# Performance work log

Hardware: AMD Instinct MI355X
Metric: run time of the kernel (lower is better)

The kernel has to match this reference:

```python
import jax, jax.numpy as jnp
import numpy as np

EMBED_DIM = 2048
NUM_HEADS = 32
NUM_KV_HEADS = 8
HEAD_DIM = EMBED_DIM // NUM_HEADS  # 64
KV_DIM = HEAD_DIM * NUM_KV_HEADS   # 512
Q_PER_KV = NUM_HEADS // NUM_KV_HEADS  # 4


def setup_inputs() -> dict:
    key = jax.random.key(0)
    ks = jax.random.split(key, 9)
    s = 1.0 / np.sqrt(EMBED_DIM)
    x = jax.random.normal(ks[0], (2, 2048, EMBED_DIM), dtype=jnp.float32)
    Wq = jax.random.uniform(ks[1], (EMBED_DIM, EMBED_DIM), jnp.float32, -s, s)
    bq = jax.random.uniform(ks[2], (EMBED_DIM,), jnp.float32, -s, s)
    Wk = jax.random.uniform(ks[3], (KV_DIM, EMBED_DIM), jnp.float32, -s, s)
    bk = jax.random.uniform(ks[4], (KV_DIM,), jnp.float32, -s, s)
    Wv = jax.random.uniform(ks[5], (KV_DIM, EMBED_DIM), jnp.float32, -s, s)
    bv = jax.random.uniform(ks[6], (KV_DIM,), jnp.float32, -s, s)
    Wo = jax.random.uniform(ks[7], (EMBED_DIM, EMBED_DIM), jnp.float32, -s, s)
    bo = jax.random.uniform(ks[8], (EMBED_DIM,), jnp.float32, -s, s)
    return {"x": x, "Wq": Wq, "bq": bq, "Wk": Wk, "bk": bk,
            "Wv": Wv, "bv": bv, "Wo": Wo, "bo": bo}


def reference(x, Wq, bq, Wk, bk, Wv, bv, Wo, bo):
    B, S, E = x.shape
    # projections (torch Linear: x @ W.T + b)
    q = x @ Wq.T + bq                       # [B,S,E]
    k = x @ Wk.T + bk                       # [B,S,KV_DIM]
    v = x @ Wv.T + bv
    # [B, num_kv, q_per_kv, S, D] and [B, num_kv, S, D] -- GQA grouping
    # avoids repeat_interleave duplication while computing identical math
    q = q.reshape(B, S, NUM_KV_HEADS, Q_PER_KV, HEAD_DIM).transpose(0, 2, 3, 1, 4)
    k = k.reshape(B, S, NUM_KV_HEADS, HEAD_DIM).transpose(0, 2, 1, 3)
    v = v.reshape(B, S, NUM_KV_HEADS, HEAD_DIM).transpose(0, 2, 1, 3)
    scale = 1.0 / np.sqrt(HEAD_DIM).astype(np.float32)
    scores = jnp.einsum('bgqsd,bgtd->bgqst', q, k) * scale  # [B,G,Qpk,S,S]
    causal = jnp.triu(jnp.ones((S, S), dtype=bool), k=1)
    scores = jnp.where(causal, jnp.float32(-jnp.inf), scores)
    attn = jax.nn.softmax(scores, axis=-1)
    out = jnp.einsum('bgqst,bgtd->bgqsd', attn, v)          # [B,G,Qpk,S,D]
    # back to [B,S,E]: head order matches repeat_interleave (kv-major)
    out = out.transpose(0, 3, 1, 2, 4).reshape(B, S, E)
    return out @ Wo.T + bo
```

## Files before the change

kernel.cpp:

```cpp
#include <hip/hip_runtime.h>
#include <stdint.h>

#define EMBED  2048
#define SEQ    2048
#define BATCH  2
#define NHEADS 32
#define NKV    8
#define HDIM   64
#define KVD    512
#define MTOT   (BATCH*SEQ)
#define QKVN   (EMBED + 2*KVD)

typedef __bf16 bf16x8 __attribute__((ext_vector_type(8)));
typedef float  f32x4  __attribute__((ext_vector_type(4)));
typedef float  f32x8v __attribute__((ext_vector_type(8)));
typedef float  f32x2v __attribute__((ext_vector_type(2)));
typedef float  f32x16 __attribute__((ext_vector_type(16)));

#define QSCALE 0.18033688f
#define M2     11.541560f

static __device__ __forceinline__ unsigned short f2bf(float f) {
    union { float f; unsigned int u; } v; v.f = f;
    return (unsigned short)((v.u + 0x7fffu + ((v.u >> 16) & 1u)) >> 16);
}

static __device__ __forceinline__ void gload_lds16(const void* g, void* l) {
    __builtin_amdgcn_global_load_lds(
        (const __attribute__((address_space(1))) void*)g,
        (__attribute__((address_space(3))) void*)l, 16, 0, 0);
}

template<int N> static __device__ __forceinline__ void waitvm() {
    if constexpr (N == 2) asm volatile("s_waitcnt vmcnt(2)" ::: "memory");
    else if constexpr (N == 3) asm volatile("s_waitcnt vmcnt(3)" ::: "memory");
    else asm volatile("s_waitcnt vmcnt(4)" ::: "memory");
}

static __device__ __forceinline__ void cast4(const float* __restrict__ in,
                                             unsigned short* __restrict__ out, int i) {
    float4 f = reinterpret_cast<const float4*>(in)[i];
    ushort4 o;
    o.x = f2bf(f.x); o.y = f2bf(f.y); o.z = f2bf(f.z); o.w = f2bf(f.w);
    reinterpret_cast<ushort4*>(out)[i] = o;
}

__global__ __launch_bounds__(256)
void prep(const float* __restrict__ x,  const float* __restrict__ Wq,
          const float* __restrict__ Wk, const float* __restrict__ Wv,
          const float* __restrict__ Wo, const float* __restrict__ bq,
          const float* __restrict__ bk, const float* __restrict__ bv,
          unsigned short* __restrict__ xb, unsigned short* __restrict__ Wqkvb,
          unsigned short* __restrict__ Wob, float* __restrict__ bqkv)
{
    const int t0 = blockIdx.x * blockDim.x + threadIdx.x;
    const int st = gridDim.x * blockDim.x;
    for (int i = t0; i < (MTOT * EMBED) / 4;  i += st) cast4(x,  xb, i);
    for (int i = t0; i < (EMBED * EMBED) / 4; i += st) cast4(Wq, Wqkvb, i);
    for (int i = t0; i < (KVD * EMBED) / 4;   i += st) cast4(Wk, Wqkvb + EMBED * EMBED, i);
    for (int i = t0; i < (KVD * EMBED) / 4;   i += st) cast4(Wv, Wqkvb + (EMBED + KVD) * EMBED, i);
    for (int i = t0; i < (EMBED * EMBED) / 4; i += st) cast4(Wo, Wob, i);
    if (t0 < QKVN / 4) {
        float4 v = (t0 < EMBED / 4) ? reinterpret_cast<const float4*>(bq)[t0]
                 : (t0 < (EMBED + KVD) / 4) ? reinterpret_cast<const float4*>(bk)[t0 - EMBED / 4]
                 : reinterpret_cast<const float4*>(bv)[t0 - (EMBED + KVD) / 4];
        reinterpret_cast<float4*>(bqkv)[t0] = v;
    }
}

__global__ __launch_bounds__(256)
void transpose_v(const unsigned short* __restrict__ qkv,
                 unsigned short* __restrict__ vt)
{
    __shared__ __align__(16) unsigned short T[64][72];
    const int bg = blockIdx.x & 15;
    const int bt = blockIdx.x >> 4;
    const int b  = bg >> 3, g = bg & 7;
    const int tid = threadIdx.x;
    const int tr  = tid >> 2, c = tid & 3;

    const unsigned short* src = qkv + ((size_t)(b * SEQ + bt * 64 + tr)) * QKVN
                              + (EMBED + KVD) + g * HDIM + c * 16;
    uint4 v0 = *reinterpret_cast<const uint4*>(src);
    uint4 v1 = *reinterpret_cast<const uint4*>(src + 8);
    *reinterpret_cast<uint4*>(&T[tr][c * 16])     = v0;
    *reinterpret_cast<uint4*>(&T[tr][c * 16 + 8]) = v1;
    __syncthreads();

    const int dr = tr;
    unsigned short o[16];
#pragma unroll
    for (int j = 0; j < 16; ++j) o[j] = T[c * 16 + j][dr];
    unsigned short* dst = vt + ((size_t)(bg * 64 + dr)) * SEQ + bt * 64 + c * 16;
    *reinterpret_cast<uint4*>(dst)     = *reinterpret_cast<uint4*>(o);
    *reinterpret_cast<uint4*>(dst + 8) = *reinterpret_cast<uint4*>(o + 8);
}

template<int WM, bool OUT_BF16>
__global__ __launch_bounds__(512, 1)
void gemm8p(const unsigned short* __restrict__ A,
            const unsigned short* __restrict__ B,
            const float* __restrict__ bias,
            void* __restrict__ C, int M, int N, int K)
{
    constexpr int BM    = WM * 32;
    constexpr int ASZ   = BM * 128;
    constexpr int BSZ   = 256 * 128;
    constexpr int AHALF = ASZ / 2;
    constexpr int AL    = AHALF / 8192;
    constexpr int BUFSZ = ASZ + BSZ;

    __shared__ __align__(16) char lds[2 * BUFSZ];

    const int tid = threadIdx.x;
    const int l   = tid & 63;
    const int w   = tid >> 6;
    const int wr  = w >> 2, wc = w & 3;
    const int lr15 = l & 15;
    const int lkb  = (l >> 4) * 16;

    const int nwg = gridDim.x;
    const int cpx = nwg >> 3;
    const int bid = blockIdx.x;
    const int swz = (bid & 7) * cpx + (bid >> 3);
    const int NMB = M / BM;
    const int m0  = (swz % NMB) * BM;
    const int n0  = (swz / NMB) * 256;

    unsigned offA[2][AL], dA[2][AL];
#pragma unroll
    for (int q = 0; q < 2; ++q)
#pragma unroll
        for (int j = 0; j < AL; ++j) {
            int L  = q * AHALF + (tid + j * 512) * 16;
            int R  = L >> 7;
            int cb = (L & 127) ^ ((R & 7) << 4);
            int lrow;
            if constexpr (WM == 8) lrow = ((R >> 6) & 1) * 128 + (R >> 7) * 64 + (R & 63);
            else                   lrow = ((R >> 5) & 1) * 64  + (R >> 6) * 32 + (R & 31);
            offA[q][j] = (unsigned)((m0 + lrow) * K * 2 + cb);
            dA[q][j]   = (unsigned)L;
        }
    unsigned offB[2][2], dB[2][2];
#pragma unroll
    for (int q = 0; q < 2; ++q)
#pragma unroll
        for (int j = 0; j < 2; ++j) {
            int L  = q * 16384 + (tid + j * 512) * 16;
            int R  = L >> 7;
            int cb = (L & 127) ^ ((R & 7) << 4);
            int lrow = ((R >> 5) & 3) * 64 + (R >> 7) * 32 + (R & 31);
            offB[q][j] = (unsigned)((n0 + lrow) * K * 2 + cb);
            dB[q][j]   = (unsigned)(ASZ + L);
        }

#define STAGE_A(q, bw, ku) { _Pragma("unroll") \
    for (int j_ = 0; j_ < AL; ++j_) \
        gload_lds16((const char*)A + offA[q][j_] + (unsigned)(ku) * 128u, (bw) + dA[q][j_]); }
#define STAGE_B(q, bw, ku) { _Pragma("unroll") \
    for (int j_ = 0; j_ < 2; ++j_) \
        gload_lds16((const char*)B + offB[q][j_] + (unsigned)(ku) * 128u, (bw) + dB[q][j_]); }

    auto rdA = [&](const char* br, int mi, int kk) -> bf16x8 {
        int row;
        if constexpr (WM == 8) row = (mi >> 2) * 128 + wr * 64 + (mi & 3) * 16 + lr15;
        else                   row = (mi >> 1) * 64  + wr * 32 + (mi & 1) * 16 + lr15;
        int byte = (row * 128 + kk * 64 + lkb) ^ ((row & 7) << 4);
        return *reinterpret_cast<const bf16x8*>(br + byte);
    };
    auto rdB = [&](const char* br, int ni, int kk) -> bf16x8 {
        int row  = (ni >> 1) * 128 + wc * 32 + (ni & 1) * 16 + lr15;
        int byte = (row * 128 + kk * 64 + lkb) ^ ((row & 7) << 4);
        return *reinterpret_cast<const bf16x8*>(br + ASZ + byte);
    };

    f32x4 acc[WM][4] = {};
    bf16x8 afr[WM / 2][2], bf0[2][2], bf1[2][2];

    STAGE_A(0, lds, 0); STAGE_B(0, lds, 0); STAGE_B(1, lds, 0); STAGE_A(1, lds, 0);
    waitvm<2 + AL>();
    __builtin_amdgcn_s_barrier();

    const int NKT = K >> 6;
    for (int u = 0; u < NKT; ++u) {
        char* br = lds + (u & 1) * BUFSZ;
        char* bw = lds + ((u & 1) ^ 1) * BUFSZ;
        const bool pf = (u + 1 < NKT);
        const int  ku = u + 1;

        if (pf) STAGE_A(0, bw, ku);
#pragma unroll
        for (int mi = 0; mi < WM / 2; ++mi)
#pragma unroll
            for (int kk = 0; kk < 2; ++kk) afr[mi][kk] = rdA(br, mi, kk);
#pragma unroll
        for (int ni = 0; ni < 2; ++ni)
#pragma unroll
            for (int kk = 0; kk < 2; ++kk) bf0[ni][kk] = rdB(br, ni, kk);
        __builtin_amdgcn_s_barrier();
        __builtin_amdgcn_s_setprio(1);
#pragma unroll
        for (int mi = 0; mi < WM / 2; ++mi)
#pragma unroll
            for (int ni = 0; ni < 2; ++ni)
#pragma unroll
                for (int kk = 0; kk < 2; ++kk)
                    acc[mi][ni] = __builtin_amdgcn_mfma_f32_16x16x32_bf16(afr[mi][kk], bf0[ni][kk], acc[mi][ni], 0, 0, 0);
        __builtin_amdgcn_s_setprio(0);
        waitvm<2 * AL>();
        __builtin_amdgcn_s_barrier();

        if (pf) STAGE_B(0, bw, ku);
#pragma unroll
        for (int ni = 0; ni < 2; ++ni)
#pragma unroll
            for (int kk = 0; kk < 2; ++kk) bf1[ni][kk] = rdB(br, 2 + ni, kk);
        __builtin_amdgcn_s_barrier();
        __builtin_amdgcn_s_setprio(1);
#pragma unroll
        for (int mi = 0; mi < WM / 2; ++mi)
#pragma unroll
            for (int ni = 0; ni < 2; ++ni)
#pragma unroll
                for (int kk = 0; kk < 2; ++kk)
                    acc[mi][2 + ni] = __builtin_amdgcn_mfma_f32_16x16x32_bf16(afr[mi][kk], bf1[ni][kk], acc[mi][2 + ni], 0, 0, 0);
        __builtin_amdgcn_s_setprio(0);
        waitvm<AL + 2>();
        __builtin_amdgcn_s_barrier();

        if (pf) STAGE_B(1, bw, ku);
#pragma unroll
        for (int mi = 0; mi < WM / 2; ++mi)
#pragma unroll
            for (int kk = 0; kk < 2; ++kk) afr[mi][kk] = rdA(br, WM / 2 + mi, kk);
        __builtin_amdgcn_s_barrier();
        __builtin_amdgcn_s_setprio(1);
#pragma unroll
        for (int mi = 0; mi < WM / 2; ++mi)
#pragma unroll
            for (int ni = 0; ni < 2; ++ni)
#pragma unroll
                for (int kk = 0; kk < 2; ++kk)
                    acc[WM / 2 + mi][ni] = __builtin_amdgcn_mfma_f32_16x16x32_bf16(afr[mi][kk], bf0[ni][kk], acc[WM / 2 + mi][ni], 0, 0, 0);
        __builtin_amdgcn_s_setprio(0);
        __builtin_amdgcn_s_barrier();

        if (pf) STAGE_A(1, bw, ku);
        __builtin_amdgcn_s_barrier();
        __builtin_amdgcn_s_setprio(1);
#pragma unroll
        for (int mi = 0; mi < WM / 2; ++mi)
#pragma unroll
            for (int ni = 0; ni < 2; ++ni)
#pragma unroll
                for (int kk = 0; kk < 2; ++kk)
                    acc[WM / 2 + mi][2 + ni] = __builtin_amdgcn_mfma_f32_16x16x32_bf16(afr[mi][kk], bf1[ni][kk], acc[WM / 2 + mi][2 + ni], 0, 0, 0);
        __builtin_amdgcn_s_setprio(0);
        waitvm<2 + AL>();
        __builtin_amdgcn_s_barrier();
    }
#undef STAGE_A
#undef STAGE_B

    float bv[4];
#pragma unroll
    for (int ni = 0; ni < 4; ++ni) bv[ni] = bias[n0 + wc * 64 + ni * 16 + lr15];
#pragma unroll
    for (int mi = 0; mi < WM; ++mi)
#pragma unroll
        for (int ni = 0; ni < 4; ++ni)
#pragma unroll
            for (int r = 0; r < 4; ++r) {
                int row = m0 + wr * (WM * 16) + mi * 16 + (l >> 4) * 4 + r;
                int col = n0 + wc * 64 + ni * 16 + lr15;
                float v = acc[mi][ni][r] + bv[ni];
                if constexpr (OUT_BF16)
                    ((unsigned short*)C)[(size_t)row * N + col] = f2bf(v);
                else
                    ((float*)C)[(size_t)row * N + col] = v;
            }
}

static __device__ __forceinline__ bf16x8 pack_frag(float p0, float p1, float p2, float p3,
                                                   float p4, float p5, float p6, float p7) {
    unsigned int w0, w1, w2, w3;
    asm("v_cvt_pk_bf16_f32 %0, %1, %2" : "=v"(w0) : "v"(p0), "v"(p1));
    asm("v_cvt_pk_bf16_f32 %0, %1, %2" : "=v"(w1) : "v"(p2), "v"(p3));
    asm("v_cvt_pk_bf16_f32 %0, %1, %2" : "=v"(w2) : "v"(p4), "v"(p5));
    asm("v_cvt_pk_bf16_f32 %0, %1, %2" : "=v"(w3) : "v"(p6), "v"(p7));
    asm("v_permlane32_swap_b32 %0, %1" : "+v"(w0), "+v"(w2));
    asm("v_permlane32_swap_b32 %0, %1" : "+v"(w1), "+v"(w3));
    union { unsigned int u[4]; bf16x8 v; } uu;
    uu.u[0] = w0; uu.u[1] = w1; uu.u[2] = w2; uu.u[3] = w3;
    return uu.v;
}

static __device__ __forceinline__ float hsum32(f32x16 a, f32x16 b) {
    f32x16 t = a + b;
    f32x8v u = __builtin_shufflevector(t, t, 0,1,2,3,4,5,6,7)
             + __builtin_shufflevector(t, t, 8,9,10,11,12,13,14,15);
    f32x4 v4 = __builtin_shufflevector(u, u, 0,1,2,3)
             + __builtin_shufflevector(u, u, 4,5,6,7);
    f32x2v v2 = __builtin_shufflevector(v4, v4, 0,1)
              + __builtin_shufflevector(v4, v4, 2,3);
    return v2[0] + v2[1];
}

__global__ __launch_bounds__(256, 2)
void gqa_attn(const unsigned short* __restrict__ qkv,
              const unsigned short* __restrict__ vtg,
              unsigned short* __restrict__ ctx)
{
    __shared__ __align__(16) unsigned short Ks[2][64 * 64];
    __shared__ __align__(16) unsigned short Vs[2][64 * 64];

    const int bid = blockIdx.x;
    const int g   = bid & 7;
    const int bh  = (bid >> 3) & 3;
    const int b   = bh >> 1;
    const int hp  = bh & 1;
    const int qt  = 31 - (bid >> 5);
    const int NT  = qt + 1;

    const int tid = threadIdx.x;
    const int l   = tid & 63;
    const int w   = tid >> 6;
    const int hi  = l >> 5;
    const int lq  = l & 31;

    const int h   = g * 4 + hp * 2 + (w >> 1);
    const int q0  = qt * 64 + (w & 1) * 32;
    const size_t rowb = (size_t)b * SEQ;
    const int kbase = EMBED + g * HDIM;

    bf16x8 qf[4];
    {
        const char* qa = (const char*)qkv + ((rowb + q0 + lq) * QKVN + (size_t)h * HDIM) * 2;
#pragma unroll
        for (int ks = 0; ks < 4; ++ks) {
            bf16x8 ta = *reinterpret_cast<const bf16x8*>(qa + (ks * 16 + hi * 8) * 2);
#pragma unroll
            for (int j = 0; j < 8; ++j)
                ta[j] = (__bf16)((float)ta[j] * QSCALE);
            qf[ks] = ta;
        }
    }

    f32x16 acc0 = {}, acc1 = {};
    float l_run = 0.0f;

    const int Lk0 = tid << 4;
    const int Lk1 = (tid + 256) << 4;
    const int Tk0 = Lk0 ^ (((Lk0 >> 7) & 7) << 4);
    const int Tk1 = Lk1 ^ (((Lk1 >> 7) & 7) << 4);
    const int kr0 = Tk0 >> 7, ko0 = Tk0 & 127;
    const int kr1 = Tk1 >> 7, ko1 = Tk1 & 127;

    const char* vtb = (const char*)vtg + (size_t)(b * 8 + g) * HDIM * SEQ * 2;

#define STAGE_KV(buf, tt) { \
    gload_lds16((const char*)qkv + ((rowb + (tt) + kr0) * QKVN + kbase) * 2 + ko0, (char*)Ks[buf] + Lk0); \
    gload_lds16((const char*)qkv + ((rowb + (tt) + kr1) * QKVN + kbase) * 2 + ko1, (char*)Ks[buf] + Lk1); \
    gload_lds16(vtb + ((size_t)kr0 * SEQ + (tt)) * 2 + ko0, (char*)Vs[buf] + Lk0); \
    gload_lds16(vtb + ((size_t)kr1 * SEQ + (tt)) * 2 + ko1, (char*)Vs[buf] + Lk1); }

    STAGE_KV(0, 0);
    __syncthreads();

    for (int kt = 0; kt < NT; ++kt) {
        const int cur = kt & 1;
        const int t0  = kt * 64;
        const bool haveNext = (kt + 1 < NT);
        if (haveNext) STAGE_KV(cur ^ 1, t0 + 64);

        const char* KsBuf = (const char*)Ks[cur];
        f32x16 s0 = {}, s1 = {};
        __builtin_amdgcn_s_setprio(1);
#pragma unroll
        for (int ks = 0; ks < 4; ++ks) {
            const int colb = (ks * 16 + hi * 8) * 2;
            int a0 = (lq * 128 + colb) ^ ((lq & 7) << 4);
            bf16x8 kf0 = *reinterpret_cast<const bf16x8*>(KsBuf + a0);
            s0 = __builtin_amdgcn_mfma_f32_32x32x16_bf16(kf0, qf[ks], s0, 0, 0, 0);
            int r1 = 32 + lq;
            int a1 = (r1 * 128 + colb) ^ ((r1 & 7) << 4);
            bf16x8 kf1 = *reinterpret_cast<const bf16x8*>(KsBuf + a1);
            s1 = __builtin_amdgcn_mfma_f32_32x32x16_bf16(kf1, qf[ks], s1, 0, 0, 0);
        }
        __builtin_amdgcn_s_setprio(0);

        if (kt == qt) {
            const int q = q0 + lq;
#pragma unroll
            for (int r = 0; r < 16; ++r) {
                int tg = t0 + (r & 3) + 8 * (r >> 2) + 4 * hi;
                if (tg > q) s0[r] = -1e30f;
                if (tg + 32 > q) s1[r] = -1e30f;
            }
        }

        s0 = s0 - M2;
        s1 = s1 - M2;
#pragma unroll
        for (int r = 0; r < 16; ++r) {
            s0[r] = __builtin_amdgcn_exp2f(s0[r]);
            s1[r] = __builtin_amdgcn_exp2f(s1[r]);
        }

        float rs = hsum32(s0, s1);
        l_run += rs + __shfl_xor(rs, 32);

        bf16x8 pa[4];
        pa[0] = pack_frag(s0[0], s0[1], s0[2], s0[3], s0[4], s0[5], s0[6], s0[7]);
        pa[1] = pack_frag(s0[8], s0[9], s0[10], s0[11], s0[12], s0[13], s0[14], s0[15]);
        pa[2] = pack_frag(s1[0], s1[1], s1[2], s1[3], s1[4], s1[5], s1[6], s1[7]);
        pa[3] = pack_frag(s1[8], s1[9], s1[10], s1[11], s1[12], s1[13], s1[14], s1[15]);

        const char* VsBuf = (const char*)Vs[cur];
        __builtin_amdgcn_s_setprio(1);
#pragma unroll
        for (int ks = 0; ks < 4; ++ks) {
            const int colb = (ks * 16 + hi * 8) * 2;
            int a0 = (lq * 128 + colb) ^ ((lq & 7) << 4);
            bf16x8 vf0 = *reinterpret_cast<const bf16x8*>(VsBuf + a0);
            acc0 = __builtin_amdgcn_mfma_f32_32x32x16_bf16(pa[ks], vf0, acc0, 0, 0, 0);
            int d1 = 32 + lq;
            int a1 = (d1 * 128 + colb) ^ ((d1 & 7) << 4);
            bf16x8 vf1 = *reinterpret_cast<const bf16x8*>(VsBuf + a1);
            acc1 = __builtin_amdgcn_mfma_f32_32x32x16_bf16(pa[ks], vf1, acc1, 0, 0, 0);
        }
        __builtin_amdgcn_s_setprio(0);

        if (haveNext) __syncthreads();
    }
#undef STAGE_KV

#pragma unroll
    for (int r = 0; r < 16; ++r) {
        int qr  = (r & 3) + 8 * (r >> 2) + 4 * hi;
        int col = h * HDIM + lq;
        float lr = __shfl(l_run, qr);
        size_t row = rowb + q0 + qr;
        ctx[row * EMBED + col]      = f2bf(acc0[r] / lr);
        ctx[row * EMBED + col + 32] = f2bf(acc1[r] / lr);
    }
}

extern "C" void kernel_launch(void* const* d_in, const int* in_sizes, int n_in,
                              void* d_out, int out_size, void* d_ws, size_t ws_size,
                              hipStream_t stream) {
    (void)in_sizes; (void)n_in; (void)out_size; (void)ws_size;
    const float* x  = (const float*)d_in[0];
    const float* Wq = (const float*)d_in[1];
    const float* bq = (const float*)d_in[2];
    const float* Wk = (const float*)d_in[3];
    const float* bk = (const float*)d_in[4];
    const float* Wv = (const float*)d_in[5];
    const float* bv = (const float*)d_in[6];
    const float* Wo = (const float*)d_in[7];
    const float* bo = (const float*)d_in[8];
    float* out = (float*)d_out;

    char* ws = (char*)d_ws;
    unsigned short* xb    = (unsigned short*)(ws);
    unsigned short* Wqkvb = (unsigned short*)(ws + 16777216);
    unsigned short* Wob   = (unsigned short*)(ws + 29360128);
    float*          bqkv  = (float*)         (ws + 37748736);
    unsigned short* QKVb  = (unsigned short*)(ws + 37761024);
    unsigned short* ctx   = (unsigned short*)(ws + 62926848);
    unsigned short* VT    = xb;

    prep<<<2048, 256, 0, stream>>>(x, Wq, Wk, Wv, Wo, bq, bk, bv,
                                   xb, Wqkvb, Wob, bqkv);

    gemm8p<8, true><<<dim3(192), 512, 0, stream>>>(
        xb, Wqkvb, bqkv, QKVb, MTOT, QKVN, EMBED);

    transpose_v<<<dim3(512), 256, 0, stream>>>(QKVb, VT);

    gqa_attn<<<dim3(1024), 256, 0, stream>>>(QKVb, VT, ctx);

    gemm8p<4, false><<<dim3(256), 512, 0, stream>>>(
        ctx, Wob, bo, out, MTOT, EMBED, EMBED);
}
```

Baseline: 170.4 us.

## Add 256x192-tile QKV GEMM kernel and trim barriers in gemm8p

Adds a new gemm192 kernel using 256x192 output tiles, so the 4096x3072 QKV projection maps onto 256 workgroups instead of 192, which fills the compute units more evenly. It uses a retuned staged double-buffered prefetch with adjusted vmcnt waits. Separately, it removes several intra-iteration s_barrier calls in gemm8p to cut synchronization stalls. Fewer barriers risk LDS read/write races between the read buffer and staged prefetch writes.

```diff
diff --git a/kernel.cpp b/kernel.cpp
--- a/kernel.cpp
+++ b/kernel.cpp
@@ -34,6 +34,7 @@
 template<int N> static __device__ __forceinline__ void waitvm() {
     if constexpr (N == 2) asm volatile("s_waitcnt vmcnt(2)" ::: "memory");
     else if constexpr (N == 3) asm volatile("s_waitcnt vmcnt(3)" ::: "memory");
+    else if constexpr (N == 5) asm volatile("s_waitcnt vmcnt(5)" ::: "memory");
     else asm volatile("s_waitcnt vmcnt(4)" ::: "memory");
 }
 
@@ -96,6 +97,181 @@
     *reinterpret_cast<uint4*>(dst + 8) = *reinterpret_cast<uint4*>(o + 8);
 }
 
+__global__ __launch_bounds__(512, 1)
+void gemm192(const unsigned short* __restrict__ A,
+             const unsigned short* __restrict__ B,
+             const float* __restrict__ bias,
+             unsigned short* __restrict__ C, int M, int N, int K)
+{
+    constexpr int ASZ   = 256 * 128;
+    constexpr int BSZ   = 192 * 128;
+    constexpr int AHALF = ASZ / 2;
+    constexpr int BUFSZ = ASZ + BSZ;
+
+    __shared__ __align__(16) char lds[2 * BUFSZ];
+
+    const int tid = threadIdx.x;
+    const int l   = tid & 63;
+    const int w   = tid >> 6;
+    const int wr  = w >> 2, wc = w & 3;
+    const int lr15 = l & 15;
+    const int lkb  = (l >> 4) * 16;
+
+    const int nwg = gridDim.x;
+    const int cpx = nwg >> 3;
+    const int bid = blockIdx.x;
+    const int swz = (bid & 7) * cpx + (bid >> 3);
+    const int NMB = M / 256;
+    const int m0  = (swz % NMB) * 256;
+    const int n0  = (swz / NMB) * 192;
+
+    unsigned offA[2][2], dA[2][2];
+#pragma unroll
+    for (int q = 0; q < 2; ++q)
+#pragma unroll
+        for (int j = 0; j < 2; ++j) {
+            int L  = q * AHALF + (tid + j * 512) * 16;
+            int R  = L >> 7;
+            int cb = (L & 127) ^ ((R & 7) << 4);
+            int lrow = ((R >> 6) & 1) * 128 + (R >> 7) * 64 + (R & 63);
+            offA[q][j] = (unsigned)((m0 + lrow) * K * 2 + cb);
+            dA[q][j]   = (unsigned)L;
+        }
+    unsigned offB[3], dB[3];
+#pragma unroll
+    for (int q = 0; q < 3; ++q) {
+        int L  = q * 8192 + tid * 16;
+        int R  = L >> 7;
+        int cb = (L & 127) ^ ((R & 7) << 4);
+        offB[q] = (unsigned)((n0 + R) * K * 2 + cb);
+        dB[q]   = (unsigned)(ASZ + L);
+    }
+
+#define STAGE_A(q, bw, ku) { _Pragma("unroll") \
+    for (int j_ = 0; j_ < 2; ++j_) \
+        gload_lds16((const char*)A + offA[q][j_] + (unsigned)(ku) * 128u, (bw) + dA[q][j_]); }
+#define STAGE_B(q, bw, ku) \
+    gload_lds16((const char*)B + offB[q] + (unsigned)(ku) * 128u, (bw) + dB[q]);
+
+    auto rdA = [&](const char* br, int mi, int kk) -> bf16x8 {
+        int row  = (mi >> 2) * 128 + wr * 64 + (mi & 3) * 16 + lr15;
+        int byte = (row * 128 + kk * 64 + lkb) ^ ((row & 7) << 4);
+        return *reinterpret_cast<const bf16x8*>(br + byte);
+    };
+    auto rdB = [&](const char* br, int ni, int kk) -> bf16x8 {
+        int row  = ni * 64 + wc * 16 + lr15;
+        int byte = (row * 128 + kk * 64 + lkb) ^ ((row & 7) << 4);
+        return *reinterpret_cast<const bf16x8*>(br + ASZ + byte);
+    };
+
+    f32x4 acc[8][3] = {};
+    bf16x8 afr[4][2], bf[3][2];
+
+    STAGE_A(0, lds, 0); STAGE_B(0, lds, 0); STAGE_B(1, lds, 0);
+    STAGE_B(2, lds, 0); STAGE_A(1, lds, 0);
+    waitvm<4>();
+    __builtin_amdgcn_s_barrier();
+
+    const int NKT = K >> 6;
+    for (int u = 0; u < NKT; ++u) {
+        char* br = lds + (u & 1) * BUFSZ;
+        char* bw = lds + ((u & 1) ^ 1) * BUFSZ;
+        const bool pf = (u + 1 < NKT);
+        const int  ku = u + 1;
+
+        if (pf) STAGE_A(0, bw, ku);
+#pragma unroll
+        for (int mi = 0; mi < 4; ++mi)
+#pragma unroll
+            for (int kk = 0; kk < 2; ++kk) afr[mi][kk] = rdA(br, mi, kk);
+#pragma unroll
+        for (int kk = 0; kk < 2; ++kk) bf[0][kk] = rdB(br, 0, kk);
+        __builtin_amdgcn_s_setprio(1);
+#pragma unroll
+        for (int mi = 0; mi < 4; ++mi)
+#pragma unroll
+            for (int kk = 0; kk < 2; ++kk)
+                acc[mi][0] = __builtin_amdgcn_mfma_f32_16x16x32_bf16(afr[mi][kk], bf[0][kk], acc[mi][0], 0, 0, 0);
+        __builtin_amdgcn_s_setprio(0);
+        waitvm<5>();
+        __builtin_amdgcn_s_barrier();
+
+        if (pf) STAGE_B(0, bw, ku);
+#pragma unroll
+        for (int kk = 0; kk < 2; ++kk) bf[1][kk] = rdB(br, 1, kk);
+        __builtin_amdgcn_s_setprio(1);
+#pragma unroll
+        for (int mi = 0; mi < 4; ++mi)
+#pragma unroll
+            for (int kk = 0; kk < 2; ++kk)
+                acc[mi][1] = __builtin_amdgcn_mfma_f32_16x16x32_bf16(afr[mi][kk], bf[1][kk], acc[mi][1], 0, 0, 0);
+        __builtin_amdgcn_s_setprio(0);
+        waitvm<5>();
+        __builtin_amdgcn_s_barrier();
+
+        if (pf) STAGE_B(1, bw, ku);
+#pragma unroll
+        for (int kk = 0; kk < 2; ++kk) bf[2][kk] = rdB(br, 2, kk);
+        __builtin_amdgcn_s_setprio(1);
+#pragma unroll
+        for (int mi = 0; mi < 4; ++mi)
+#pragma unroll
+            for (int kk = 0; kk < 2; ++kk)
+                acc[mi][2] = __builtin_amdgcn_mfma_f32_16x16x32_bf16(afr[mi][kk], bf[2][kk], acc[mi][2], 0, 0, 0);
+        __builtin_amdgcn_s_setprio(0);
+        waitvm<4>();
+        __builtin_amdgcn_s_barrier();
+
+        if (pf) STAGE_B(2, bw, ku);
+#pragma unroll
+        for (int mi = 0; mi < 4; ++mi)
+#pragma unroll
+            for (int kk = 0; kk < 2; ++kk) afr[mi][kk] = rdA(br, 4 + mi, kk);
+        __builtin_amdgcn_s_setprio(1);
+#pragma unroll
+        for (int mi = 0; mi < 4; ++mi)
+#pragma unroll
+            for (int kk = 0; kk < 2; ++kk)
+                acc[4 + mi][0] = __builtin_amdgcn_mfma_f32_16x16x32_bf16(afr[mi][kk], bf[0][kk], acc[4 + mi][0], 0, 0, 0);
+        __builtin_amdgcn_s_setprio(0);
+
+        if (pf) STAGE_A(1, bw, ku);
+        __builtin_amdgcn_s_setprio(1);
+#pragma unroll
+        for (int mi = 0; mi < 4; ++mi)
+#pragma unroll
+            for (int kk = 0; kk < 2; ++kk)
+                acc[4 + mi][1] = __builtin_amdgcn_mfma_f32_16x16x32_bf16(afr[mi][kk], bf[1][kk], acc[4 + mi][1], 0, 0, 0);
+        __builtin_amdgcn_s_setprio(0);
+
+        __builtin_amdgcn_s_setprio(1);
+#pragma unroll
+        for (int mi = 0; mi < 4; ++mi)
+#pragma unroll
+            for (int kk = 0; kk < 2; ++kk)
+                acc[4 + mi][2] = __builtin_amdgcn_mfma_f32_16x16x32_bf16(afr[mi][kk], bf[2][kk], acc[4 + mi][2], 0, 0, 0);
+        __builtin_amdgcn_s_setprio(0);
+        waitvm<4>();
+        __builtin_amdgcn_s_barrier();
+    }
+#undef STAGE_A
+#undef STAGE_B
+
+    float bv[3];
+#pragma unroll
+    for (int ni = 0; ni < 3; ++ni) bv[ni] = bias[n0 + ni * 64 + wc * 16 + lr15];
+#pragma unroll
+    for (int mi = 0; mi < 8; ++mi)
+#pragma unroll
+        for (int ni = 0; ni < 3; ++ni)
+#pragma unroll
+            for (int r = 0; r < 4; ++r) {
+                int row = m0 + wr * 128 + mi * 16 + (l >> 4) * 4 + r;
+                int col = n0 + ni * 64 + wc * 16 + lr15;
+                C[(size_t)row * N + col] = f2bf(acc[mi][ni][r] + bv[ni]);
+            }
+}
+
 template<int WM, bool OUT_BF16>
 __global__ __launch_bounds__(512, 1)
 void gemm8p(const unsigned short* __restrict__ A,
@@ -197,7 +373,6 @@
         for (int ni = 0; ni < 2; ++ni)
 #pragma unroll
             for (int kk = 0; kk < 2; ++kk) bf0[ni][kk] = rdB(br, ni, kk);
-        __builtin_amdgcn_s_barrier();
         __builtin_amdgcn_s_setprio(1);
 #pragma unroll
         for (int mi = 0; mi < WM / 2; ++mi)
@@ -215,7 +390,6 @@
         for (int ni = 0; ni < 2; ++ni)
 #pragma unroll
             for (int kk = 0; kk < 2; ++kk) bf1[ni][kk] = rdB(br, 2 + ni, kk);
-        __builtin_amdgcn_s_barrier();
         __builtin_amdgcn_s_setprio(1);
 #pragma unroll
         for (int mi = 0; mi < WM / 2; ++mi)
@@ -233,7 +407,6 @@
         for (int mi = 0; mi < WM / 2; ++mi)
 #pragma unroll
             for (int kk = 0; kk < 2; ++kk) afr[mi][kk] = rdA(br, WM / 2 + mi, kk);
-        __builtin_amdgcn_s_barrier();
         __builtin_amdgcn_s_setprio(1);
 #pragma unroll
         for (int mi = 0; mi < WM / 2; ++mi)
@@ -243,10 +416,8 @@
                 for (int kk = 0; kk < 2; ++kk)
                     acc[WM / 2 + mi][ni] = __builtin_amdgcn_mfma_f32_16x16x32_bf16(afr[mi][kk], bf0[ni][kk], acc[WM / 2 + mi][ni], 0, 0, 0);
         __builtin_amdgcn_s_setprio(0);
-        __builtin_amdgcn_s_barrier();
 
         if (pf) STAGE_A(1, bw, ku);
-        __builtin_amdgcn_s_barrier();
         __builtin_amdgcn_s_setprio(1);
 #pragma unroll
         for (int mi = 0; mi < WM / 2; ++mi)
@@ -473,7 +644,7 @@
     prep<<<2048, 256, 0, stream>>>(x, Wq, Wk, Wv, Wo, bq, bk, bv,
                                    xb, Wqkvb, Wob, bqkv);
 
-    gemm8p<8, true><<<dim3(192), 512, 0, stream>>>(
+    gemm192<<<dim3(256), 512, 0, stream>>>(
         xb, Wqkvb, bqkv, QKVb, MTOT, QKVN, EMBED);
 
     transpose_v<<<dim3(512), 256, 0, stream>>>(QKVb, VT);
```

Result: faster. 164.6 us (-3.4%).
